# Performance work log

Hardware: AMD Instinct MI355X
Metric: run time of the kernel (lower is better)

The kernel has to match this reference:

```python
import jax, jax.numpy as jnp
import numpy as np

EPS = 1e-8  # F.cosine_similarity default eps


def setup_inputs() -> dict:
    key = jax.random.key(0)
    k1, k2, k3 = jax.random.split(key, 3)
    C, S, Q, D_IN, Z_DIM = 256, 5, 64, 1024, 128
    xs = jax.random.normal(k1, (C, S, D_IN), dtype=jnp.float32)
    xq = jax.random.normal(k2, (C, Q, D_IN), dtype=jnp.float32)
    W = jax.random.normal(k3, (D_IN, Z_DIM), dtype=jnp.float32) / np.sqrt(D_IN)
    return {"xs": xs, "xq": xq, "W": W}


def _protonet_loss(xs, xq, W):
    C, S, D = xs.shape
    Q = xq.shape[1]
    # encoder (linear) applied to concatenated support+query, as in the original
    x = jnp.concatenate([xs.reshape(C * S, D), xq.reshape(C * Q, D)], axis=0)
    z = x @ W                                   # [C*(S+Q), Zd]
    Zd = z.shape[-1]
    z_proto = z[: C * S].reshape(C, S, Zd).mean(axis=1)   # [C, Zd]
    zq = z[C * S:]                                        # [C*Q, Zd]
    # squared euclidean distance (GEMM form, avoids [CQ, C, Zd] intermediate)
    d2 = (jnp.sum(zq * zq, axis=-1, keepdims=True)
          + jnp.sum(z_proto * z_proto, axis=-1)[None, :]
          - 2.0 * (zq @ z_proto.T))                       # [C*Q, C]
    lp = d2.reshape(C, Q, C)                              # label_predicts
    # leave-one-out: for each class i drop column i -> [C, Q, C-1]
    loo_idx = np.stack([np.delete(np.arange(C), i) for i in range(C)])  # [C, C-1]
    idx = jnp.broadcast_to(jnp.asarray(loo_idx)[:, None, :], (C, Q, C - 1))
    loo = jnp.take_along_axis(lp, idx, axis=2)            # [C, Q, C-1]
    # pairwise cosine similarity between query rows j<k, per class
    nrm = jnp.maximum(jnp.linalg.norm(loo, axis=-1), EPS)
    a = loo / nrm[..., None]
    sim = jnp.einsum('cqd,ckd->cqk', a, a)                # [C, Q, Q]
    pair_mask = jnp.triu(jnp.ones((Q, Q), dtype=bool), 1)
    n_pairs = C * (Q * (Q - 1) // 2)
    cos_loss = jnp.sum(jnp.where(pair_mask[None], sim, 0.0)) / n_pairs
    # log_softmax over prototype axis; accuracy vs diagonal targets
    log_p_y = jax.nn.log_softmax(-d2, axis=1).reshape(C, Q, C)
    y_hat = jnp.argmax(log_p_y, axis=2)                   # [C, Q]
    acc = jnp.mean((y_hat == jnp.arange(C)[:, None]).astype(jnp.float32))
    # original overwrites loss_val with the cosine-similarity loss
    return cos_loss, acc


def reference(xs, xq, W):
    return _protonet_loss(xs, xq, W)
```

## Files before the change

kernel.cpp:

```cpp
#include <hip/hip_runtime.h>


typedef __attribute__((ext_vector_type(8))) short s8v;
typedef __attribute__((ext_vector_type(4))) float f32x4;

__device__ __forceinline__ short f2bf(float f) {
  union { float f; unsigned u; } v; v.f = f;
  unsigned r = (v.u + 0x7fffu + ((v.u >> 16) & 1u)) >> 16;
  return (short)r;
}

__global__ __launch_bounds__(256) void k_prep(
    const float* __restrict__ xs, const float* __restrict__ W,
    float* __restrict__ xbar, unsigned short* __restrict__ Wt,
    float* __restrict__ out) {
  __shared__ unsigned short T[128 * 68];
  const int tid = threadIdx.x;
  if (blockIdx.x < 256) {
    const int c = blockIdx.x;
    if (c == 0 && tid < 2) out[tid] = 0.0f;
    const float* b = xs + (size_t)c * 5120;
    for (int e = tid; e < 1024; e += 256) {
      float s = b[e] + b[1024 + e] + b[2048 + e] + b[3072 + e] + b[4096 + e];
      xbar[(size_t)c * 1024 + e] = s * 0.2f;
    }
  } else {
    const int kb = (blockIdx.x - 256) * 64;
#pragma unroll
    for (int s = 0; s < 8; ++s) {
      int idx = tid + s * 256;
      int kr = idx >> 5, n4 = idx & 31;
      float4 v = *(const float4*)(W + (size_t)(kb + kr) * 128 + n4 * 4);
      T[(n4 * 4 + 0) * 68 + kr] = (unsigned short)f2bf(v.x);
      T[(n4 * 4 + 1) * 68 + kr] = (unsigned short)f2bf(v.y);
      T[(n4 * 4 + 2) * 68 + kr] = (unsigned short)f2bf(v.z);
      T[(n4 * 4 + 3) * 68 + kr] = (unsigned short)f2bf(v.w);
    }
    __syncthreads();
#pragma unroll
    for (int s = 0; s < 8; ++s) {
      int idx = tid + s * 256;
      int n = idx >> 4, k4 = idx & 15;
      ushort4 o;
      o.x = T[n * 68 + k4 * 4 + 0];
      o.y = T[n * 68 + k4 * 4 + 1];
      o.z = T[n * 68 + k4 * 4 + 2];
      o.w = T[n * 68 + k4 * 4 + 3];
      *(ushort4*)(Wt + (size_t)n * 1024 + kb + k4 * 4) = o;
    }
  }
}

__global__ __launch_bounds__(64, 1) void k_gemm_z(
    const float* __restrict__ xbar, const float* __restrict__ xq,
    const unsigned short* __restrict__ Wt,
    unsigned short* __restrict__ zb, float* __restrict__ n2) {
  const int rb = blockIdx.x * 16;
  const int lane = threadIdx.x & 63, ln = lane & 15, q = lane >> 4;
  const float* abase = (rb < 256) ? (xbar + (size_t)rb * 1024)
                                  : (xq + (size_t)(rb - 256) * 1024);
  const float* arow = abase + (size_t)ln * 1024 + q * 8;
  const unsigned short* brow = Wt + (size_t)ln * 1024 + q * 8;
  f32x4 acc[8] = {};
  float4 a0[2], a1[2];
  s8v bfr[2][8];
  a0[0] = *(const float4*)(arow + 0);
  a1[0] = *(const float4*)(arow + 4);
  a0[1] = *(const float4*)(arow + 32);
  a1[1] = *(const float4*)(arow + 36);
#pragma unroll
  for (int t = 0; t < 8; ++t)
    bfr[0][t] = *(const s8v*)(brow + (size_t)t * 16 * 1024);
#pragma unroll
  for (int kt = 0; kt < 32; ++kt) {
    const int cur = kt & 1;
    if (kt < 31) {
#pragma unroll
      for (int t = 0; t < 8; ++t)
        bfr[cur ^ 1][t] =
            *(const s8v*)(brow + (size_t)t * 16 * 1024 + (kt + 1) * 32);
    }
    s8v af = { f2bf(a0[cur].x), f2bf(a0[cur].y), f2bf(a0[cur].z), f2bf(a0[cur].w),
               f2bf(a1[cur].x), f2bf(a1[cur].y), f2bf(a1[cur].z), f2bf(a1[cur].w) };
    if (kt < 30) {
      a0[cur] = *(const float4*)(arow + (kt + 2) * 32);
      a1[cur] = *(const float4*)(arow + (kt + 2) * 32 + 4);
    }
#pragma unroll
    for (int t = 0; t < 8; ++t)
      acc[t] = __builtin_amdgcn_mfma_f32_16x16x32_bf16(af, bfr[cur][t], acc[t], 0, 0, 0);
  }
#pragma unroll
  for (int p = 0; p < 4; ++p) {
    int grow = rb + q * 4 + p;
    float sp = 0.0f;
#pragma unroll
    for (int t = 0; t < 8; ++t) {
      float v = acc[t][p];
      zb[(size_t)grow * 128 + t * 16 + ln] = (unsigned short)f2bf(v);
      sp += v * v;
    }
    sp += __shfl_xor(sp, 1);
    sp += __shfl_xor(sp, 2);
    sp += __shfl_xor(sp, 4);
    sp += __shfl_xor(sp, 8);
    if (ln == 0) n2[grow] = sp;
  }
}

__global__ __launch_bounds__(256, 1) void k_d2red(
    const unsigned short* __restrict__ zb, const float* __restrict__ n2,
    float* __restrict__ out) {
  __shared__ float Dt[256 * 65];
  __shared__ float rv[256];
  __shared__ int   ri[256];
  __shared__ float rss[256];
  __shared__ float invn[64];
  __shared__ float sred[4];
  __shared__ float s_tc, s_aq2, s_corr;
  const int tid = threadIdx.x;
  const int c = blockIdx.x;
  const int w = tid >> 6, lane = tid & 63, ln = lane & 15, qd = lane >> 4;

  f32x4 acc[16] = {};
  const unsigned short* Az = zb + (size_t)(256 + c * 64 + w * 16 + ln) * 128;
#pragma unroll
  for (int kt = 0; kt < 4; ++kt) {
    s8v af = *(const s8v*)(Az + kt * 32 + qd * 8);
#pragma unroll
    for (int t = 0; t < 16; ++t) {
      s8v bf = *(const s8v*)(zb + (size_t)(t * 16 + ln) * 128 + kt * 32 + qd * 8);
      acc[t] = __builtin_amdgcn_mfma_f32_16x16x32_bf16(af, bf, acc[t], 0, 0, 0);
    }
  }
#pragma unroll
  for (int p = 0; p < 4; ++p) {
    int qloc = w * 16 + qd * 4 + p;
    float qn = n2[256 + c * 64 + qloc];
#pragma unroll
    for (int t = 0; t < 16; ++t) {
      int j = t * 16 + ln;
      Dt[j * 65 + qloc] = qn + n2[j] - 2.0f * acc[t][p];
    }
  }
  __syncthreads();

  {
    const int q = tid & 63, jb = (tid >> 6) * 64;
    float mn = 3.4e38f; int mi = 0; float ss = 0.0f;
    for (int jj = 0; jj < 64; ++jj) {
      int j = jb + jj;
      float f = Dt[j * 65 + q];
      ss += f * f;
      if (f < mn) { mn = f; mi = j; }
    }
    rv[tid] = mn; ri[tid] = mi; rss[tid] = ss;
  }
  __syncthreads();
  if (tid < 64) {
    float bm = rv[tid]; int bi = ri[tid]; float ss = rss[tid];
    for (int h = 1; h < 4; ++h) {
      float v = rv[h * 64 + tid];
      ss += rss[h * 64 + tid];
      if (v < bm) { bm = v; bi = ri[h * 64 + tid]; }
    }
    float col = Dt[c * 65 + tid];
    float loo2 = fmaxf(ss - col * col, 0.0f);
    float nrm = fmaxf(sqrtf(loo2), 1e-8f);
    float inv = 1.0f / nrm;
    invn[tid] = inv;
    float aq2 = loo2 * inv * inv;
    float corr = (bi == c) ? 1.0f : 0.0f;
    for (int m = 1; m < 64; m <<= 1) {
      aq2 += __shfl_xor(aq2, m);
      corr += __shfl_xor(corr, m);
    }
    if (tid == 0) { s_aq2 = aq2; s_corr = corr; }
  }
  __syncthreads();
  float t = 0.0f;
  for (int qq = 0; qq < 64; ++qq) t += Dt[tid * 65 + qq] * invn[qq];
  if (tid == c) s_tc = t;
  float t2 = t * t;
  for (int m = 1; m < 64; m <<= 1) t2 += __shfl_xor(t2, m);
  if ((tid & 63) == 0) sred[tid >> 6] = t2;
  __syncthreads();
  if (tid == 0) {
    float S2 = sred[0] + sred[1] + sred[2] + sred[3];
    float bs = 0.5f * (S2 - s_tc * s_tc - s_aq2);
    atomicAdd(&out[0], bs * (1.0f / 516096.0f));
    atomicAdd(&out[1], s_corr * (1.0f / 16384.0f));
  }
}

extern "C" void kernel_launch(void* const* d_in, const int* in_sizes, int n_in,
                              void* d_out, int out_size, void* d_ws, size_t ws_size,
                              hipStream_t stream) {
  const float* xs = (const float*)d_in[0];
  const float* xq = (const float*)d_in[1];
  const float* W  = (const float*)d_in[2];
  float* out = (float*)d_out;

  float* ws = (float*)d_ws;
  float* xbar = ws;
  unsigned short* Wt = (unsigned short*)(xbar + 262144);
  unsigned short* zb = Wt + 131072;
  float* n2 = (float*)(zb + (size_t)16640 * 128);

  k_prep<<<dim3(272), dim3(256), 0, stream>>>(xs, W, xbar, Wt, out);
  k_gemm_z<<<dim3(1040), dim3(64), 0, stream>>>(xbar, xq, Wt, zb, n2);
  k_d2red<<<dim3(256), dim3(256), 0, stream>>>(zb, n2, out);
}
```

Measured before the change: 152.8 us.

## Share W tile across four waves via double-buffered LDS in z GEMM

The z GEMM now uses 256-thread blocks covering 64 rows instead of one wave per 16 rows. Each wave loads a quarter of the bf16 W k-slice into a double-buffered shared-memory tile, and all four waves read B fragments from LDS. This cuts redundant global/L2 reads of W by four and reduces register pressure from the per-wave B prefetch. In exchange it adds a block barrier every k-step, and the grid shrinks to 260 blocks, which may leave some CUs idle.

```diff
diff --git a/kernel.cpp b/kernel.cpp
--- a/kernel.cpp
+++ b/kernel.cpp
@@ -51,34 +51,49 @@
   }
 }
 
-__global__ __launch_bounds__(64, 1) void k_gemm_z(
+__global__ __launch_bounds__(256)
+__attribute__((amdgpu_waves_per_eu(1, 2))) void k_gemm_z(
     const float* __restrict__ xbar, const float* __restrict__ xq,
     const unsigned short* __restrict__ Wt,
     unsigned short* __restrict__ zb, float* __restrict__ n2) {
-  const int rb = blockIdx.x * 16;
-  const int lane = threadIdx.x & 63, ln = lane & 15, q = lane >> 4;
+  __shared__ short Bs[2][4096];
+  const int tid = threadIdx.x;
+  const int w = tid >> 6, l = tid & 63, ln = l & 15, qd = l >> 4;
+  const int rb = blockIdx.x * 64;
   const float* abase = (rb < 256) ? (xbar + (size_t)rb * 1024)
                                   : (xq + (size_t)(rb - 256) * 1024);
-  const float* arow = abase + (size_t)ln * 1024 + q * 8;
-  const unsigned short* brow = Wt + (size_t)ln * 1024 + q * 8;
+  const float* arow = abase + (size_t)(w * 16 + ln) * 1024 + qd * 8;
+  const int tg0 = 2 * w, tg1 = 2 * w + 1;
+  const unsigned short* bsrc0 = Wt + (size_t)(tg0 * 16 + ln) * 1024 + qd * 8;
+  const unsigned short* bsrc1 = Wt + (size_t)(tg1 * 16 + ln) * 1024 + qd * 8;
+  short* bdst0 = &Bs[0][tg0 * 512 + l * 8];
+  short* bdst1 = &Bs[0][tg1 * 512 + l * 8];
+
   f32x4 acc[8] = {};
   float4 a0[2], a1[2];
-  s8v bfr[2][8];
+  s8v bn0, bn1;
+
+  bn0 = *(const s8v*)(bsrc0);
+  bn1 = *(const s8v*)(bsrc1);
   a0[0] = *(const float4*)(arow + 0);
   a1[0] = *(const float4*)(arow + 4);
   a0[1] = *(const float4*)(arow + 32);
   a1[1] = *(const float4*)(arow + 36);
-#pragma unroll
-  for (int t = 0; t < 8; ++t)
-    bfr[0][t] = *(const s8v*)(brow + (size_t)t * 16 * 1024);
-#pragma unroll
+  *(s8v*)bdst0 = bn0;
+  *(s8v*)bdst1 = bn1;
+  bn0 = *(const s8v*)(bsrc0 + 32);
+  bn1 = *(const s8v*)(bsrc1 + 32);
+
   for (int kt = 0; kt < 32; ++kt) {
     const int cur = kt & 1;
+    __syncthreads();
     if (kt < 31) {
-#pragma unroll
-      for (int t = 0; t < 8; ++t)
-        bfr[cur ^ 1][t] =
-            *(const s8v*)(brow + (size_t)t * 16 * 1024 + (kt + 1) * 32);
+      *(s8v*)(bdst0 + (cur ^ 1) * 4096) = bn0;
+      *(s8v*)(bdst1 + (cur ^ 1) * 4096) = bn1;
+      if (kt < 30) {
+        bn0 = *(const s8v*)(bsrc0 + (kt + 2) * 32);
+        bn1 = *(const s8v*)(bsrc1 + (kt + 2) * 32);
+      }
     }
     s8v af = { f2bf(a0[cur].x), f2bf(a0[cur].y), f2bf(a0[cur].z), f2bf(a0[cur].w),
                f2bf(a1[cur].x), f2bf(a1[cur].y), f2bf(a1[cur].z), f2bf(a1[cur].w) };
@@ -87,12 +102,14 @@
       a1[cur] = *(const float4*)(arow + (kt + 2) * 32 + 4);
     }
 #pragma unroll
-    for (int t = 0; t < 8; ++t)
-      acc[t] = __builtin_amdgcn_mfma_f32_16x16x32_bf16(af, bfr[cur][t], acc[t], 0, 0, 0);
+    for (int t = 0; t < 8; ++t) {
+      s8v bf = *(const s8v*)&Bs[cur][t * 512 + l * 8];
+      acc[t] = __builtin_amdgcn_mfma_f32_16x16x32_bf16(af, bf, acc[t], 0, 0, 0);
+    }
   }
 #pragma unroll
   for (int p = 0; p < 4; ++p) {
-    int grow = rb + q * 4 + p;
+    int grow = rb + w * 16 + qd * 4 + p;
     float sp = 0.0f;
 #pragma unroll
     for (int t = 0; t < 8; ++t) {
@@ -208,6 +225,6 @@
   float* n2 = (float*)(zb + (size_t)16640 * 128);
 
   k_prep<<<dim3(272), dim3(256), 0, stream>>>(xs, W, xbar, Wt, out);
-  k_gemm_z<<<dim3(1040), dim3(64), 0, stream>>>(xbar, xq, Wt, zb, n2);
+  k_gemm_z<<<dim3(260), dim3(256), 0, stream>>>(xbar, xq, Wt, zb, n2);
   k_d2red<<<dim3(256), dim3(256), 0, stream>>>(zb, n2, out);
 }
```

New measurement: 144.6 us. 5.4% less time.

## Restructure z GEMM into 8-wave blocks with shared-memory W tiles and split-K

Applied to the files above, without the earlier changes.

The z projection GEMM now runs 512-thread blocks that each cover 64 rows instead of one 64-thread wave per 16 rows. The bf16 W tile is staged through double-buffered LDS and shared by four row-group waves. Each row group is split across two waves that handle the two halves of K, with partial sums combined through LDS before writing z and its squared norms. The aim is to cut redundant global reads of W across waves and add K-parallelism, at the cost of block syncs and fewer blocks in the grid (260 vs 1040).

```diff
diff --git a/kernel.cpp b/kernel.cpp
--- a/kernel.cpp
+++ b/kernel.cpp
@@ -51,60 +51,116 @@
   }
 }
 
-__global__ __launch_bounds__(64, 1) void k_gemm_z(
+__global__ __launch_bounds__(512, 2) void k_gemm_z(
     const float* __restrict__ xbar, const float* __restrict__ xq,
     const unsigned short* __restrict__ Wt,
     unsigned short* __restrict__ zb, float* __restrict__ n2) {
-  const int rb = blockIdx.x * 16;
-  const int lane = threadIdx.x & 63, ln = lane & 15, q = lane >> 4;
+  __shared__ short Bs[2][2][2][4096];
+  const int tid = threadIdx.x;
+  const int w = tid >> 6, l = tid & 63, ln = l & 15, qd = l >> 4;
+  const int rg = w >> 1, h = w & 1;
+  const int rb = blockIdx.x * 64;
   const float* abase = (rb < 256) ? (xbar + (size_t)rb * 1024)
                                   : (xq + (size_t)(rb - 256) * 1024);
-  const float* arow = abase + (size_t)ln * 1024 + q * 8;
-  const unsigned short* brow = Wt + (size_t)ln * 1024 + q * 8;
+  const float* arow = abase + (size_t)(rg * 16 + ln) * 1024 + h * 512 + qd * 8;
+  const int scol = ((tid >> 6) << 4) + (tid & 15);
+  const int sk8 = (tid >> 4) & 3;
+  const unsigned short* wsrc = Wt + (size_t)scol * 1024 + sk8 * 8;
+
   f32x4 acc[8] = {};
-  float4 a0[2], a1[2];
-  s8v bfr[2][8];
-  a0[0] = *(const float4*)(arow + 0);
-  a1[0] = *(const float4*)(arow + 4);
-  a0[1] = *(const float4*)(arow + 32);
-  a1[1] = *(const float4*)(arow + 36);
-#pragma unroll
-  for (int t = 0; t < 8; ++t)
-    bfr[0][t] = *(const s8v*)(brow + (size_t)t * 16 * 1024);
-#pragma unroll
-  for (int kt = 0; kt < 32; ++kt) {
-    const int cur = kt & 1;
-    if (kt < 31) {
+  s8v breg[4];
+  float4 areg[2][4];
+
+#pragma unroll
+  for (int pl = 0; pl < 4; ++pl) {
+    int hh = pl >> 1, ss = pl & 1;
+    *(s8v*)&Bs[0][hh][ss][tid * 8] =
+        *(const s8v*)(wsrc + hh * 512 + ss * 32);
+  }
+#pragma unroll
+  for (int pl = 0; pl < 4; ++pl) {
+    int hh = pl >> 1, ss = pl & 1;
+    breg[pl] = *(const s8v*)(wsrc + hh * 512 + ss * 32 + 64);
+  }
+  areg[0][0] = *(const float4*)(arow + 0);
+  areg[0][1] = *(const float4*)(arow + 4);
+  areg[0][2] = *(const float4*)(arow + 32);
+  areg[0][3] = *(const float4*)(arow + 36);
+  areg[1][0] = *(const float4*)(arow + 64);
+  areg[1][1] = *(const float4*)(arow + 68);
+  areg[1][2] = *(const float4*)(arow + 96);
+  areg[1][3] = *(const float4*)(arow + 100);
+
+  for (int kt = 0; kt < 8; ++kt) {
+    const int buf = kt & 1;
+    __syncthreads();
+    if (kt < 7) {
+#pragma unroll
+      for (int pl = 0; pl < 4; ++pl) {
+        int hh = pl >> 1, ss = pl & 1;
+        *(s8v*)&Bs[buf ^ 1][hh][ss][tid * 8] = breg[pl];
+      }
+      if (kt < 6) {
+#pragma unroll
+        for (int pl = 0; pl < 4; ++pl) {
+          int hh = pl >> 1, ss = pl & 1;
+          breg[pl] = *(const s8v*)(wsrc + hh * 512 + ss * 32 + (kt + 2) * 64);
+        }
+      }
+    }
+    s8v af0 = { f2bf(areg[buf][0].x), f2bf(areg[buf][0].y),
+                f2bf(areg[buf][0].z), f2bf(areg[buf][0].w),
+                f2bf(areg[buf][1].x), f2bf(areg[buf][1].y),
+                f2bf(areg[buf][1].z), f2bf(areg[buf][1].w) };
+    s8v af1 = { f2bf(areg[buf][2].x), f2bf(areg[buf][2].y),
+                f2bf(areg[buf][2].z), f2bf(areg[buf][2].w),
+                f2bf(areg[buf][3].x), f2bf(areg[buf][3].y),
+                f2bf(areg[buf][3].z), f2bf(areg[buf][3].w) };
+    if (kt < 6) {
+      areg[buf][0] = *(const float4*)(arow + (kt + 2) * 64);
+      areg[buf][1] = *(const float4*)(arow + (kt + 2) * 64 + 4);
+      areg[buf][2] = *(const float4*)(arow + (kt + 2) * 64 + 32);
+      areg[buf][3] = *(const float4*)(arow + (kt + 2) * 64 + 36);
+    }
+#pragma unroll
+    for (int t = 0; t < 8; ++t) {
+      s8v bf = *(const s8v*)&Bs[buf][h][0][t * 512 + l * 8];
+      acc[t] = __builtin_amdgcn_mfma_f32_16x16x32_bf16(af0, bf, acc[t], 0, 0, 0);
+    }
+#pragma unroll
+    for (int t = 0; t < 8; ++t) {
+      s8v bf = *(const s8v*)&Bs[buf][h][1][t * 512 + l * 8];
+      acc[t] = __builtin_amdgcn_mfma_f32_16x16x32_bf16(af1, bf, acc[t], 0, 0, 0);
+    }
+  }
+
+  __syncthreads();
+  float* R = (float*)&Bs[0][0][0][0];
+  if (h == 1) {
+#pragma unroll
+    for (int p = 0; p < 4; ++p)
 #pragma unroll
       for (int t = 0; t < 8; ++t)
-        bfr[cur ^ 1][t] =
-            *(const s8v*)(brow + (size_t)t * 16 * 1024 + (kt + 1) * 32);
-    }
-    s8v af = { f2bf(a0[cur].x), f2bf(a0[cur].y), f2bf(a0[cur].z), f2bf(a0[cur].w),
-               f2bf(a1[cur].x), f2bf(a1[cur].y), f2bf(a1[cur].z), f2bf(a1[cur].w) };
-    if (kt < 30) {
-      a0[cur] = *(const float4*)(arow + (kt + 2) * 32);
-      a1[cur] = *(const float4*)(arow + (kt + 2) * 32 + 4);
-    }
-#pragma unroll
-    for (int t = 0; t < 8; ++t)
-      acc[t] = __builtin_amdgcn_mfma_f32_16x16x32_bf16(af, bfr[cur][t], acc[t], 0, 0, 0);
-  }
-#pragma unroll
-  for (int p = 0; p < 4; ++p) {
-    int grow = rb + q * 4 + p;
-    float sp = 0.0f;
-#pragma unroll
-    for (int t = 0; t < 8; ++t) {
-      float v = acc[t][p];
-      zb[(size_t)grow * 128 + t * 16 + ln] = (unsigned short)f2bf(v);
-      sp += v * v;
-    }
-    sp += __shfl_xor(sp, 1);
-    sp += __shfl_xor(sp, 2);
-    sp += __shfl_xor(sp, 4);
-    sp += __shfl_xor(sp, 8);
-    if (ln == 0) n2[grow] = sp;
+        R[rg * 2112 + (qd * 4 + p) * 132 + t * 16 + ln] = acc[t][p];
+  }
+  __syncthreads();
+  if (h == 0) {
+#pragma unroll
+    for (int p = 0; p < 4; ++p) {
+      int grow = rb + rg * 16 + qd * 4 + p;
+      float sp = 0.0f;
+#pragma unroll
+      for (int t = 0; t < 8; ++t) {
+        float v = acc[t][p] + R[rg * 2112 + (qd * 4 + p) * 132 + t * 16 + ln];
+        zb[(size_t)grow * 128 + t * 16 + ln] = (unsigned short)f2bf(v);
+        sp += v * v;
+      }
+      sp += __shfl_xor(sp, 1);
+      sp += __shfl_xor(sp, 2);
+      sp += __shfl_xor(sp, 4);
+      sp += __shfl_xor(sp, 8);
+      if (ln == 0) n2[grow] = sp;
+    }
   }
 }
 
@@ -159,10 +215,10 @@
   __syncthreads();
   if (tid < 64) {
     float bm = rv[tid]; int bi = ri[tid]; float ss = rss[tid];
-    for (int h = 1; h < 4; ++h) {
-      float v = rv[h * 64 + tid];
-      ss += rss[h * 64 + tid];
-      if (v < bm) { bm = v; bi = ri[h * 64 + tid]; }
+    for (int hh = 1; hh < 4; ++hh) {
+      float v = rv[hh * 64 + tid];
+      ss += rss[hh * 64 + tid];
+      if (v < bm) { bm = v; bi = ri[hh * 64 + tid]; }
     }
     float col = Dt[c * 65 + tid];
     float loo2 = fmaxf(ss - col * col, 0.0f);
@@ -208,6 +264,6 @@
   float* n2 = (float*)(zb + (size_t)16640 * 128);
 
   k_prep<<<dim3(272), dim3(256), 0, stream>>>(xs, W, xbar, Wt, out);
-  k_gemm_z<<<dim3(1040), dim3(64), 0, stream>>>(xbar, xq, Wt, zb, n2);
+  k_gemm_z<<<dim3(260), dim3(512), 0, stream>>>(xbar, xq, Wt, zb, n2);
   k_d2red<<<dim3(256), dim3(256), 0, stream>>>(zb, n2, out);
 }
```

New measurement: 141.1 us. -7.7%, faster.

## Split GEMM K dimension across four waves with LDS reduction

Applied to the files above, without the earlier changes.

The z-projection GEMM moves from one wave per 16-row block to four waves per block. Each wave handles a quarter of the K=1024 reduction, and the partial results are summed through shared memory. This is meant to raise parallelism and latency hiding for a memory-bound GEMM with only 1040 single-wave blocks. The output is written as 16-byte vector stores from the reduced tile. The cost is an extra LDS round trip plus a barrier, and the prefetch is now only one step deep.

```diff
diff --git a/kernel.cpp b/kernel.cpp
--- a/kernel.cpp
+++ b/kernel.cpp
@@ -51,60 +51,74 @@
   }
 }
 
-__global__ __launch_bounds__(64, 1) void k_gemm_z(
+__global__ __launch_bounds__(256) void k_gemm_z(
     const float* __restrict__ xbar, const float* __restrict__ xq,
     const unsigned short* __restrict__ Wt,
     unsigned short* __restrict__ zb, float* __restrict__ n2) {
+  __shared__ float R[4][16][132];
+  const int tid = threadIdx.x;
+  const int w = tid >> 6, l = tid & 63, ln = l & 15, qd = l >> 4;
   const int rb = blockIdx.x * 16;
-  const int lane = threadIdx.x & 63, ln = lane & 15, q = lane >> 4;
   const float* abase = (rb < 256) ? (xbar + (size_t)rb * 1024)
                                   : (xq + (size_t)(rb - 256) * 1024);
-  const float* arow = abase + (size_t)ln * 1024 + q * 8;
-  const unsigned short* brow = Wt + (size_t)ln * 1024 + q * 8;
+  const float* arow = abase + (size_t)ln * 1024 + w * 256 + qd * 8;
+  const unsigned short* bbase = Wt + (size_t)ln * 1024 + w * 256 + qd * 8;
+
   f32x4 acc[8] = {};
-  float4 a0[2], a1[2];
-  s8v bfr[2][8];
-  a0[0] = *(const float4*)(arow + 0);
-  a1[0] = *(const float4*)(arow + 4);
-  a0[1] = *(const float4*)(arow + 32);
-  a1[1] = *(const float4*)(arow + 36);
+  float4 a0c = *(const float4*)(arow + 0);
+  float4 a1c = *(const float4*)(arow + 4);
+  s8v bc[8];
 #pragma unroll
   for (int t = 0; t < 8; ++t)
-    bfr[0][t] = *(const s8v*)(brow + (size_t)t * 16 * 1024);
-#pragma unroll
-  for (int kt = 0; kt < 32; ++kt) {
-    const int cur = kt & 1;
-    if (kt < 31) {
+    bc[t] = *(const s8v*)(bbase + (size_t)t * 16384);
+
+#pragma unroll
+  for (int kt = 0; kt < 8; ++kt) {
+    float4 a0n, a1n;
+    s8v bn[8];
+    if (kt < 7) {
+      a0n = *(const float4*)(arow + (kt + 1) * 32);
+      a1n = *(const float4*)(arow + (kt + 1) * 32 + 4);
 #pragma unroll
       for (int t = 0; t < 8; ++t)
-        bfr[cur ^ 1][t] =
-            *(const s8v*)(brow + (size_t)t * 16 * 1024 + (kt + 1) * 32);
-    }
-    s8v af = { f2bf(a0[cur].x), f2bf(a0[cur].y), f2bf(a0[cur].z), f2bf(a0[cur].w),
-               f2bf(a1[cur].x), f2bf(a1[cur].y), f2bf(a1[cur].z), f2bf(a1[cur].w) };
-    if (kt < 30) {
-      a0[cur] = *(const float4*)(arow + (kt + 2) * 32);
-      a1[cur] = *(const float4*)(arow + (kt + 2) * 32 + 4);
-    }
+        bn[t] = *(const s8v*)(bbase + (size_t)t * 16384 + (kt + 1) * 32);
+    }
+    s8v af = { f2bf(a0c.x), f2bf(a0c.y), f2bf(a0c.z), f2bf(a0c.w),
+               f2bf(a1c.x), f2bf(a1c.y), f2bf(a1c.z), f2bf(a1c.w) };
 #pragma unroll
     for (int t = 0; t < 8; ++t)
-      acc[t] = __builtin_amdgcn_mfma_f32_16x16x32_bf16(af, bfr[cur][t], acc[t], 0, 0, 0);
-  }
-#pragma unroll
-  for (int p = 0; p < 4; ++p) {
-    int grow = rb + q * 4 + p;
+      acc[t] = __builtin_amdgcn_mfma_f32_16x16x32_bf16(af, bc[t], acc[t], 0, 0, 0);
+    if (kt < 7) {
+      a0c = a0n; a1c = a1n;
+#pragma unroll
+      for (int t = 0; t < 8; ++t) bc[t] = bn[t];
+    }
+  }
+
+#pragma unroll
+  for (int p = 0; p < 4; ++p)
+#pragma unroll
+    for (int t = 0; t < 8; ++t)
+      R[w][qd * 4 + p][t * 16 + ln] = acc[t][p];
+  __syncthreads();
+  {
+    const int r = tid >> 4, cc = (tid & 15) * 8;
+    float v[8];
+#pragma unroll
+    for (int e = 0; e < 8; ++e)
+      v[e] = R[0][r][cc + e] + R[1][r][cc + e] + R[2][r][cc + e] + R[3][r][cc + e];
+    s8v o = { f2bf(v[0]), f2bf(v[1]), f2bf(v[2]), f2bf(v[3]),
+              f2bf(v[4]), f2bf(v[5]), f2bf(v[6]), f2bf(v[7]) };
+    const int grow = rb + r;
+    *(s8v*)&zb[(size_t)grow * 128 + cc] = o;
     float sp = 0.0f;
 #pragma unroll
-    for (int t = 0; t < 8; ++t) {
-      float v = acc[t][p];
-      zb[(size_t)grow * 128 + t * 16 + ln] = (unsigned short)f2bf(v);
-      sp += v * v;
-    }
+    for (int e = 0; e < 8; ++e) sp += v[e] * v[e];
     sp += __shfl_xor(sp, 1);
     sp += __shfl_xor(sp, 2);
     sp += __shfl_xor(sp, 4);
     sp += __shfl_xor(sp, 8);
-    if (ln == 0) n2[grow] = sp;
+    if ((tid & 15) == 0) n2[grow] = sp;
   }
 }
 
@@ -159,10 +173,10 @@
   __syncthreads();
   if (tid < 64) {
     float bm = rv[tid]; int bi = ri[tid]; float ss = rss[tid];
-    for (int h = 1; h < 4; ++h) {
-      float v = rv[h * 64 + tid];
-      ss += rss[h * 64 + tid];
-      if (v < bm) { bm = v; bi = ri[h * 64 + tid]; }
+    for (int hh = 1; hh < 4; ++hh) {
+      float v = rv[hh * 64 + tid];
+      ss += rss[hh * 64 + tid];
+      if (v < bm) { bm = v; bi = ri[hh * 64 + tid]; }
     }
     float col = Dt[c * 65 + tid];
     float loo2 = fmaxf(ss - col * col, 0.0f);
@@ -208,6 +222,6 @@
   float* n2 = (float*)(zb + (size_t)16640 * 128);
 
   k_prep<<<dim3(272), dim3(256), 0, stream>>>(xs, W, xbar, Wt, out);
-  k_gemm_z<<<dim3(1040), dim3(64), 0, stream>>>(xbar, xq, Wt, zb, n2);
+  k_gemm_z<<<dim3(1040), dim3(256), 0, stream>>>(xbar, xq, Wt, zb, n2);
   k_d2red<<<dim3(256), dim3(256), 0, stream>>>(zb, n2, out);
 }
```

Result: no change. 152.7 us (-0.1%).
